# Performance work log

Hardware: AMD Instinct MI355X
Metric: run time of the kernel (lower is better)

Reference implementation:

```python
import jax, jax.numpy as jnp
import numpy as np

VOCAB = 100000
DIM = 128
B = 16384
C_MAX = 10
K_NEG = 5


def setup_inputs() -> dict:
    key = jax.random.key(0)
    k1, k2, k3, k4, k5, k6 = jax.random.split(key, 6)
    bound = 0.5 / DIM
    return {
        "target_words": jax.random.randint(k1, (B,), 0, VOCAB),
        "context_words": jax.random.randint(k2, (B, C_MAX), 0, VOCAB),
        "context_lens": jax.random.randint(k3, (B,), 0, C_MAX + 1),
        "negative_words": jax.random.randint(k4, (B, K_NEG), 0, VOCAB),
        # input embeddings init: uniform(-0.5/dim, 0.5/dim); output init zeros in the
        # original, but we use small random values so gradients/scores are non-trivial.
        "in_emb": jax.random.uniform(k5, (VOCAB, DIM), jnp.float32, -bound, bound),
        "out_emb": jax.random.normal(k6, (VOCAB, DIM), jnp.float32) * 0.01,
    }


def reference(target_words, context_words, context_lens, negative_words, in_emb, out_emb):
    t = in_emb[target_words]                      # (B, D)
    c = out_emb[context_words]                    # (B, C, D)
    n = out_emb[negative_words]                   # (B, K, D)

    pos_scores = jnp.einsum("bd,bcd->bc", t, c)   # (B, C)
    neg_scores = jnp.einsum("bd,bkd->bk", t, n)   # (B, K)

    mask = (jnp.arange(C_MAX)[None, :] < context_lens[:, None]).astype(t.dtype)
    lens = context_lens.astype(t.dtype)
    has_ctx = lens > 0

    # per-sample mean of -logsigmoid over valid contexts; skip samples with 0 contexts
    pos_per = -jnp.sum(jax.nn.log_sigmoid(pos_scores) * mask, axis=1)
    pos_per = jnp.where(has_ctx, pos_per / jnp.maximum(lens, 1.0), 0.0)

    neg_per = -jnp.mean(jax.nn.log_sigmoid(-neg_scores), axis=1)
    neg_per = jnp.where(has_ctx, neg_per, 0.0)    # original `continue` skips negatives too

    positive_loss = jnp.sum(pos_per) / B
    negative_loss = jnp.sum(neg_per) / B
    return positive_loss, negative_loss
```

## Files before the change

### kernel.cpp

```cpp
#include <hip/hip_runtime.h>
#include <math.h>
#include <stdint.h>

#define VOCAB 100000
#define DIM   128
#define BATCH 16384
#define CMAX  10
#define KNEG  5

typedef float f32x4 __attribute__((ext_vector_type(4)));

__device__ __forceinline__ float log_sigmoid(float x) {
    return fminf(x, 0.0f) - log1pf(expf(-fabsf(x)));
}

#define DPP_ADD_STEP(v, ctrl)                                                  \
    v += __int_as_float(__builtin_amdgcn_update_dpp(                           \
        0, __float_as_int(v), (ctrl), 0xF, 0xF, false))

__device__ __forceinline__ float dpp_reduce32_to_lane31(float v) {
    DPP_ADD_STEP(v, 0x111);
    DPP_ADD_STEP(v, 0x112);
    DPP_ADD_STEP(v, 0x114);
    DPP_ADD_STEP(v, 0x118);
    DPP_ADD_STEP(v, 0x142);
    return v;
}

__global__ __launch_bounds__(256) void score_loss_kernel(
    const int*   __restrict__ tgt,
    const int*   __restrict__ ctx,
    const int*   __restrict__ lens,
    const int*   __restrict__ neg,
    const float* __restrict__ in_emb,
    const float* __restrict__ out_emb,
    float2*      __restrict__ per_sample,
    float*       __restrict__ out)
{
    const int tid  = threadIdx.x;
    const int lane = tid & 63;
    const int sub  = lane & 31;
    const int half = lane >> 5;
    const int b    = (blockIdx.x * 256 + tid) >> 6;

    if (blockIdx.x == 0 && tid < 2) out[tid] = 0.0f;

    const int len    = lens[b];
    const int t_word = tgt[b];
    int words[8];
#pragma unroll
    for (int jj = 0; jj < 8; ++jj) {
        const int j = half * 8 + jj;
        if (j < CMAX)             words[jj] = ctx[b * CMAX + j];
        else if (j < CMAX + KNEG) words[jj] = neg[b * KNEG + (j - CMAX)];
        else                      words[jj] = 0;
    }

    asm volatile("s_waitcnt vmcnt(0)" ::: "memory");

    const uint32_t sub16 = (uint32_t)sub * 16u;
    f32x4 tv;
    {
        uint32_t off = (uint32_t)t_word * (DIM * 4u) + sub16;
        asm volatile("global_load_dwordx4 %0, %1, %2"
                     : "=v"(tv) : "v"(off), "s"(in_emb));
    }
    f32x4 rv[8];
#pragma unroll
    for (int jj = 0; jj < 8; ++jj) {
        uint32_t off = (uint32_t)words[jj] * (DIM * 4u) + sub16;
        asm volatile("global_load_dwordx4 %0, %1, %2"
                     : "=v"(rv[jj]) : "v"(off), "s"(out_emb));
    }

    float p[8];
#pragma unroll
    for (int jj = 0; jj < 8; ++jj) {
        asm volatile("s_waitcnt vmcnt(%[cnt])"
                     : "+v"(rv[jj]), "+v"(tv)
                     : [cnt] "i"(7 - jj)
                     : "memory");
        float d = tv.x * rv[jj].x + tv.y * rv[jj].y +
                  tv.z * rv[jj].z + tv.w * rv[jj].w;
        p[jj] = dpp_reduce32_to_lane31(d);
    }

    float bc[8];
#pragma unroll
    for (int jj = 0; jj < 8; ++jj) bc[jj] = __shfl(p[jj], 31, 32);

    const int sel = sub & 7;
    float a0 = (sel & 1) ? bc[1] : bc[0];
    float a1 = (sel & 1) ? bc[3] : bc[2];
    float a2 = (sel & 1) ? bc[5] : bc[4];
    float a3 = (sel & 1) ? bc[7] : bc[6];
    float b0 = (sel & 2) ? a1 : a0;
    float b1 = (sel & 2) ? a3 : a2;
    float s  = (sel & 4) ? b1 : b0;

    const int  j        = half * 8 + sel;
    const bool neg_slot = (j >= CMAX) && (j < CMAX + KNEG);
    const bool active   = (sub < 8);

    float v    = log_sigmoid(neg_slot ? -s : s);
    float posc = (active && j < len)    ? v : 0.0f;
    float negc = (active && neg_slot)   ? v : 0.0f;

    posc += __shfl_xor(posc, 1, 64);
    posc += __shfl_xor(posc, 2, 64);
    posc += __shfl_xor(posc, 4, 64);
    posc += __shfl_xor(posc, 32, 64);
    negc += __shfl_xor(negc, 1, 64);
    negc += __shfl_xor(negc, 2, 64);
    negc += __shfl_xor(negc, 4, 64);
    negc += __shfl_xor(negc, 32, 64);

    if (lane == 0) {
        float2 r;
        if (len > 0) {
            r.x = -posc / (float)len;
            r.y = -negc * (1.0f / KNEG);
        } else {
            r.x = 0.0f;
            r.y = 0.0f;
        }
        per_sample[b] = r;
    }
}

__global__ __launch_bounds__(256) void reduce_kernel(
    const float2* __restrict__ per_sample,
    float*        __restrict__ out)
{
    const int tid = threadIdx.x;
    const int b   = blockIdx.x * 256 + tid;

    const float2 pr = per_sample[b];
    float pos = pr.x;
    float neg = pr.y;

#pragma unroll
    for (int m = 32; m >= 1; m >>= 1) {
        pos += __shfl_xor(pos, m, 64);
        neg += __shfl_xor(neg, m, 64);
    }
    __shared__ float s_pos[4];
    __shared__ float s_neg[4];
    const int wave = tid >> 6;
    if ((tid & 63) == 0) { s_pos[wave] = pos; s_neg[wave] = neg; }
    __syncthreads();
    if (tid == 0) {
        float ps = s_pos[0] + s_pos[1] + s_pos[2] + s_pos[3];
        float ns = s_neg[0] + s_neg[1] + s_neg[2] + s_neg[3];
        atomicAdd(&out[0], ps * (1.0f / BATCH));
        atomicAdd(&out[1], ns * (1.0f / BATCH));
    }
}

extern "C" void kernel_launch(void* const* d_in, const int* in_sizes, int n_in,
                              void* d_out, int out_size, void* d_ws, size_t ws_size,
                              hipStream_t stream) {
    const int*   tgt     = (const int*)  d_in[0];
    const int*   ctx     = (const int*)  d_in[1];
    const int*   lens    = (const int*)  d_in[2];
    const int*   neg     = (const int*)  d_in[3];
    const float* in_emb  = (const float*)d_in[4];
    const float* out_emb = (const float*)d_in[5];
    float* out          = (float*)d_out;
    float2* per_sample  = (float2*)d_ws;

    score_loss_kernel<<<BATCH / 4, 256, 0, stream>>>(
        tgt, ctx, lens, neg, in_emb, out_emb, per_sample, out);

    reduce_kernel<<<BATCH / 256, 256, 0, stream>>>(per_sample, out);
}
```

Measured before the change: 132.0 us.

## Gather only valid context rows and use full-wave dwordx2 row loads

Each wave now loads only the len valid context rows plus the negatives. Samples with zero contexts skip all loads, since the reference zeroes their loss anyway. Previously the wave always fetched all ten context rows and the five negatives. Each embedding row is now read by the whole 64-lane wave with dwordx2 loads, and the dot product is reduced with a 64-lane DPP chain instead of two half-waves using dwordx4. The aim is to cut gather traffic on masked rows, in exchange for a single full wait on all loads instead of the staggered per-row waits and a longer reduction per row.

```diff
diff --git a/kernel.cpp b/kernel.cpp
--- a/kernel.cpp
+++ b/kernel.cpp
@@ -7,8 +7,9 @@
 #define BATCH 16384
 #define CMAX  10
 #define KNEG  5
+#define RMAX  (CMAX + KNEG)
 
-typedef float f32x4 __attribute__((ext_vector_type(4)));
+typedef float f32x2 __attribute__((ext_vector_type(2)));
 
 __device__ __forceinline__ float log_sigmoid(float x) {
     return fminf(x, 0.0f) - log1pf(expf(-fabsf(x)));
@@ -18,12 +19,13 @@
     v += __int_as_float(__builtin_amdgcn_update_dpp(                           \
         0, __float_as_int(v), (ctrl), 0xF, 0xF, false))
 
-__device__ __forceinline__ float dpp_reduce32_to_lane31(float v) {
+__device__ __forceinline__ float dpp_reduce64_to_lane63(float v) {
     DPP_ADD_STEP(v, 0x111);
     DPP_ADD_STEP(v, 0x112);
     DPP_ADD_STEP(v, 0x114);
     DPP_ADD_STEP(v, 0x118);
     DPP_ADD_STEP(v, 0x142);
+    DPP_ADD_STEP(v, 0x143);
     return v;
 }
 
@@ -39,93 +41,97 @@
 {
     const int tid  = threadIdx.x;
     const int lane = tid & 63;
-    const int sub  = lane & 31;
-    const int half = lane >> 5;
     const int b    = (blockIdx.x * 256 + tid) >> 6;
 
     if (blockIdx.x == 0 && tid < 2) out[tid] = 0.0f;
 
-    const int len    = lens[b];
-    const int t_word = tgt[b];
-    int words[8];
+    const int len = lens[b];
+    float2 res; res.x = 0.0f; res.y = 0.0f;
+
+    if (len > 0) {
+        const int R      = len + KNEG;
+        const int t_word = tgt[b];
+
+        int words[RMAX];
 #pragma unroll
-    for (int jj = 0; jj < 8; ++jj) {
-        const int j = half * 8 + jj;
-        if (j < CMAX)             words[jj] = ctx[b * CMAX + j];
-        else if (j < CMAX + KNEG) words[jj] = neg[b * KNEG + (j - CMAX)];
-        else                      words[jj] = 0;
+        for (int j = 0; j < RMAX; ++j) {
+            if (j < R) {
+                const int cj = (j < CMAX) ? j : (CMAX - 1);
+                int nj = j - len;
+                nj = (nj < 0) ? 0 : ((nj > KNEG - 1) ? (KNEG - 1) : nj);
+                words[j] = (j < len) ? ctx[b * CMAX + cj]
+                                     : neg[b * KNEG + nj];
+            }
+        }
+
+        const uint32_t lane8 = (uint32_t)lane * 8u;
+        f32x2 tv;
+        asm volatile("global_load_dwordx2 %0, %1, %2"
+                     : "=v"(tv)
+                     : "v"((uint32_t)t_word * (DIM * 4u) + lane8),
+                       "s"(in_emb));
+        f32x2 rv[RMAX];
+#pragma unroll
+        for (int j = 0; j < RMAX; ++j) {
+            if (j < R) {
+                asm volatile("global_load_dwordx2 %0, %1, %2"
+                             : "=v"(rv[j])
+                             : "v"((uint32_t)words[j] * (DIM * 4u) + lane8),
+                               "s"(out_emb));
+            }
+        }
+        asm volatile("s_waitcnt vmcnt(0)" ::: "memory");
+        __builtin_amdgcn_sched_barrier(0);
+
+        float bc[RMAX];
+#pragma unroll
+        for (int j = 0; j < RMAX; ++j) bc[j] = 0.0f;
+#pragma unroll
+        for (int j = 0; j < RMAX; ++j) {
+            if (j < R) {
+                float d = tv.x * rv[j].x + tv.y * rv[j].y;
+                float s = dpp_reduce64_to_lane63(d);
+                bc[j] = __shfl(s, 63, 64);
+            }
+        }
+
+        const int sel = lane & 15;
+        float m0 = (sel & 1) ? bc[1]  : bc[0];
+        float m1 = (sel & 1) ? bc[3]  : bc[2];
+        float m2 = (sel & 1) ? bc[5]  : bc[4];
+        float m3 = (sel & 1) ? bc[7]  : bc[6];
+        float m4 = (sel & 1) ? bc[9]  : bc[8];
+        float m5 = (sel & 1) ? bc[11] : bc[10];
+        float m6 = (sel & 1) ? bc[13] : bc[12];
+        float m7 = (sel & 1) ? 0.0f   : bc[14];
+        float n0 = (sel & 2) ? m1 : m0;
+        float n1 = (sel & 2) ? m3 : m2;
+        float n2 = (sel & 2) ? m5 : m4;
+        float n3 = (sel & 2) ? m7 : m6;
+        float q0 = (sel & 4) ? n1 : n0;
+        float q1 = (sel & 4) ? n3 : n2;
+        float sv = (sel & 8) ? q1 : q0;
+
+        const bool active = (lane < 16) && (sel < R);
+        const bool is_neg = (sel >= len);
+        float v = log_sigmoid(is_neg ? -sv : sv);
+        float posc = (active && !is_neg) ? v : 0.0f;
+        float negc = (active &&  is_neg) ? v : 0.0f;
+
+        posc += __shfl_xor(posc, 1, 64);
+        posc += __shfl_xor(posc, 2, 64);
+        posc += __shfl_xor(posc, 4, 64);
+        posc += __shfl_xor(posc, 8, 64);
+        negc += __shfl_xor(negc, 1, 64);
+        negc += __shfl_xor(negc, 2, 64);
+        negc += __shfl_xor(negc, 4, 64);
+        negc += __shfl_xor(negc, 8, 64);
+
+        res.x = -posc / (float)len;
+        res.y = -negc * (1.0f / KNEG);
     }
 
-    asm volatile("s_waitcnt vmcnt(0)" ::: "memory");
-
-    const uint32_t sub16 = (uint32_t)sub * 16u;
-    f32x4 tv;
-    {
-        uint32_t off = (uint32_t)t_word * (DIM * 4u) + sub16;
-        asm volatile("global_load_dwordx4 %0, %1, %2"
-                     : "=v"(tv) : "v"(off), "s"(in_emb));
-    }
-    f32x4 rv[8];
-#pragma unroll
-    for (int jj = 0; jj < 8; ++jj) {
-        uint32_t off = (uint32_t)words[jj] * (DIM * 4u) + sub16;
-        asm volatile("global_load_dwordx4 %0, %1, %2"
-                     : "=v"(rv[jj]) : "v"(off), "s"(out_emb));
-    }
-
-    float p[8];
-#pragma unroll
-    for (int jj = 0; jj < 8; ++jj) {
-        asm volatile("s_waitcnt vmcnt(%[cnt])"
-                     : "+v"(rv[jj]), "+v"(tv)
-                     : [cnt] "i"(7 - jj)
-                     : "memory");
-        float d = tv.x * rv[jj].x + tv.y * rv[jj].y +
-                  tv.z * rv[jj].z + tv.w * rv[jj].w;
-        p[jj] = dpp_reduce32_to_lane31(d);
-    }
-
-    float bc[8];
-#pragma unroll
-    for (int jj = 0; jj < 8; ++jj) bc[jj] = __shfl(p[jj], 31, 32);
-
-    const int sel = sub & 7;
-    float a0 = (sel & 1) ? bc[1] : bc[0];
-    float a1 = (sel & 1) ? bc[3] : bc[2];
-    float a2 = (sel & 1) ? bc[5] : bc[4];
-    float a3 = (sel & 1) ? bc[7] : bc[6];
-    float b0 = (sel & 2) ? a1 : a0;
-    float b1 = (sel & 2) ? a3 : a2;
-    float s  = (sel & 4) ? b1 : b0;
-
-    const int  j        = half * 8 + sel;
-    const bool neg_slot = (j >= CMAX) && (j < CMAX + KNEG);
-    const bool active   = (sub < 8);
-
-    float v    = log_sigmoid(neg_slot ? -s : s);
-    float posc = (active && j < len)    ? v : 0.0f;
-    float negc = (active && neg_slot)   ? v : 0.0f;
-
-    posc += __shfl_xor(posc, 1, 64);
-    posc += __shfl_xor(posc, 2, 64);
-    posc += __shfl_xor(posc, 4, 64);
-    posc += __shfl_xor(posc, 32, 64);
-    negc += __shfl_xor(negc, 1, 64);
-    negc += __shfl_xor(negc, 2, 64);
-    negc += __shfl_xor(negc, 4, 64);
-    negc += __shfl_xor(negc, 32, 64);
-
-    if (lane == 0) {
-        float2 r;
-        if (len > 0) {
-            r.x = -posc / (float)len;
-            r.y = -negc * (1.0f / KNEG);
-        } else {
-            r.x = 0.0f;
-            r.y = 0.0f;
-        }
-        per_sample[b] = r;
-    }
+    if (lane == 0) per_sample[b] = res;
 }
 
 __global__ __launch_bounds__(256) void reduce_kernel(
```

After: 253.4 us. 92.0% more time.

## Process four samples per wave with double-buffered gather loads

Applied to the files above, without the earlier changes.

Each wave now handles four samples instead of one and keeps two sets of embedding-row loads in flight, consuming one set while the next is issued. Index loads become wave-uniform, so they can go through the scalar path. Unused context slots are redirected to a negative-word row that is already being fetched, so those loads should hit cache. The grid shrinks by a factor of four, which trades occupancy-based latency hiding for explicit in-wave pipelining and raises register pressure.

```diff
diff --git a/kernel.cpp b/kernel.cpp
--- a/kernel.cpp
+++ b/kernel.cpp
@@ -26,6 +26,103 @@
     DPP_ADD_STEP(v, 0x142);
     return v;
 }
+
+
+#define ISSUE(twv, w, tv, rv)                                                  \
+    {                                                                          \
+        asm volatile("global_load_dwordx4 %0, %1, %2"                          \
+                     : "=v"(tv)                                                \
+                     : "v"((uint32_t)(twv) * 512u + sub16), "s"(in_emb));      \
+        asm volatile("global_load_dwordx4 %0, %1, %2"                          \
+                     : "=v"(rv[0])                                             \
+                     : "v"((uint32_t)(w)[0] * 512u + sub16), "s"(out_emb));    \
+        asm volatile("global_load_dwordx4 %0, %1, %2"                          \
+                     : "=v"(rv[1])                                             \
+                     : "v"((uint32_t)(w)[1] * 512u + sub16), "s"(out_emb));    \
+        asm volatile("global_load_dwordx4 %0, %1, %2"                          \
+                     : "=v"(rv[2])                                             \
+                     : "v"((uint32_t)(w)[2] * 512u + sub16), "s"(out_emb));    \
+        asm volatile("global_load_dwordx4 %0, %1, %2"                          \
+                     : "=v"(rv[3])                                             \
+                     : "v"((uint32_t)(w)[3] * 512u + sub16), "s"(out_emb));    \
+        asm volatile("global_load_dwordx4 %0, %1, %2"                          \
+                     : "=v"(rv[4])                                             \
+                     : "v"((uint32_t)(w)[4] * 512u + sub16), "s"(out_emb));    \
+        asm volatile("global_load_dwordx4 %0, %1, %2"                          \
+                     : "=v"(rv[5])                                             \
+                     : "v"((uint32_t)(w)[5] * 512u + sub16), "s"(out_emb));    \
+        asm volatile("global_load_dwordx4 %0, %1, %2"                          \
+                     : "=v"(rv[6])                                             \
+                     : "v"((uint32_t)(w)[6] * 512u + sub16), "s"(out_emb));    \
+        asm volatile("global_load_dwordx4 %0, %1, %2"                          \
+                     : "=v"(rv[7])                                             \
+                     : "v"((uint32_t)(w)[7] * 512u + sub16), "s"(out_emb));    \
+    }
+
+#define WAITN(n, tv, rv)                                                       \
+    asm volatile("s_waitcnt vmcnt(" #n ")"                                     \
+                 : "+v"(tv), "+v"(rv[0]), "+v"(rv[1]), "+v"(rv[2]),            \
+                   "+v"(rv[3]), "+v"(rv[4]), "+v"(rv[5]), "+v"(rv[6]),         \
+                   "+v"(rv[7])                                                 \
+                 :                                                             \
+                 : "memory")
+
+#define BUILD_WORDS(i, w)                                                      \
+    {                                                                          \
+        _Pragma("unroll")                                                      \
+        for (int jj = 0; jj < 8; ++jj) {                                       \
+            const int w0 = (jj < len_[i]) ? cw_[i][jj] : nw_[i][0];            \
+            int w1;                                                            \
+            if (jj < 2)      w1 = ((8 + jj) < len_[i]) ? cw_[i][8 + jj]        \
+                                                       : nw_[i][0];            \
+            else if (jj < 7) w1 = nw_[i][jj - 2];                              \
+            else             w1 = nw_[i][0];                                   \
+            (w)[jj] = half ? w1 : w0;                                          \
+        }                                                                      \
+    }
+
+#define CONSUME(tv, rv, len, res)                                              \
+    {                                                                          \
+        float p[8];                                                            \
+        _Pragma("unroll")                                                      \
+        for (int jj = 0; jj < 8; ++jj) {                                       \
+            float d = tv.x * rv[jj].x + tv.y * rv[jj].y +                      \
+                      tv.z * rv[jj].z + tv.w * rv[jj].w;                       \
+            p[jj] = dpp_reduce32_to_lane31(d);                                 \
+        }                                                                      \
+        float bc[8];                                                           \
+        _Pragma("unroll")                                                      \
+        for (int jj = 0; jj < 8; ++jj) bc[jj] = __shfl(p[jj], 31, 32);         \
+        const int sel = sub & 7;                                               \
+        float a0 = (sel & 1) ? bc[1] : bc[0];                                  \
+        float a1 = (sel & 1) ? bc[3] : bc[2];                                  \
+        float a2 = (sel & 1) ? bc[5] : bc[4];                                  \
+        float a3 = (sel & 1) ? bc[7] : bc[6];                                  \
+        float b0_ = (sel & 2) ? a1 : a0;                                       \
+        float b1_ = (sel & 2) ? a3 : a2;                                       \
+        float sv = (sel & 4) ? b1_ : b0_;                                      \
+        const int  j        = half * 8 + sel;                                  \
+        const bool neg_slot = (j >= CMAX) && (j < CMAX + KNEG);                \
+        const bool active   = (sub < 8);                                       \
+        float v    = log_sigmoid(neg_slot ? -sv : sv);                         \
+        float posc = (active && j < (len)) ? v : 0.0f;                         \
+        float negc = (active && neg_slot)  ? v : 0.0f;                         \
+        posc += __shfl_xor(posc, 1, 64);                                       \
+        posc += __shfl_xor(posc, 2, 64);                                       \
+        posc += __shfl_xor(posc, 4, 64);                                       \
+        posc += __shfl_xor(posc, 32, 64);                                      \
+        negc += __shfl_xor(negc, 1, 64);                                       \
+        negc += __shfl_xor(negc, 2, 64);                                       \
+        negc += __shfl_xor(negc, 4, 64);                                       \
+        negc += __shfl_xor(negc, 32, 64);                                      \
+        if ((len) > 0) {                                                       \
+            res.x = -posc / (float)(len);                                      \
+            res.y = -negc * (1.0f / KNEG);                                     \
+        } else {                                                               \
+            res.x = 0.0f;                                                      \
+            res.y = 0.0f;                                                      \
+        }                                                                      \
+    }
 
 __global__ __launch_bounds__(256) void score_loss_kernel(
     const int*   __restrict__ tgt,
@@ -41,90 +138,53 @@
     const int lane = tid & 63;
     const int sub  = lane & 31;
     const int half = lane >> 5;
-    const int b    = (blockIdx.x * 256 + tid) >> 6;
+    const int wid  = __builtin_amdgcn_readfirstlane((blockIdx.x * 256 + tid) >> 6);
+    const int b0   = wid * 4;
 
     if (blockIdx.x == 0 && tid < 2) out[tid] = 0.0f;
 
-    const int len    = lens[b];
-    const int t_word = tgt[b];
-    int words[8];
-#pragma unroll
-    for (int jj = 0; jj < 8; ++jj) {
-        const int j = half * 8 + jj;
-        if (j < CMAX)             words[jj] = ctx[b * CMAX + j];
-        else if (j < CMAX + KNEG) words[jj] = neg[b * KNEG + (j - CMAX)];
-        else                      words[jj] = 0;
-    }
+    int len_[4], tw_[4];
+    int cw_[4][CMAX], nw_[4][KNEG];
+#pragma unroll
+    for (int i = 0; i < 4; ++i) {
+        len_[i] = lens[b0 + i];
+        tw_[i]  = tgt[b0 + i];
+#pragma unroll
+        for (int c = 0; c < CMAX; ++c) cw_[i][c] = ctx[(b0 + i) * CMAX + c];
+#pragma unroll
+        for (int k = 0; k < KNEG; ++k) nw_[i][k] = neg[(b0 + i) * KNEG + k];
+    }
+
+    const uint32_t sub16 = (uint32_t)sub * 16u;
 
     asm volatile("s_waitcnt vmcnt(0)" ::: "memory");
 
-    const uint32_t sub16 = (uint32_t)sub * 16u;
-    f32x4 tv;
-    {
-        uint32_t off = (uint32_t)t_word * (DIM * 4u) + sub16;
-        asm volatile("global_load_dwordx4 %0, %1, %2"
-                     : "=v"(tv) : "v"(off), "s"(in_emb));
-    }
-    f32x4 rv[8];
-#pragma unroll
-    for (int jj = 0; jj < 8; ++jj) {
-        uint32_t off = (uint32_t)words[jj] * (DIM * 4u) + sub16;
-        asm volatile("global_load_dwordx4 %0, %1, %2"
-                     : "=v"(rv[jj]) : "v"(off), "s"(out_emb));
-    }
-
-    float p[8];
-#pragma unroll
-    for (int jj = 0; jj < 8; ++jj) {
-        asm volatile("s_waitcnt vmcnt(%[cnt])"
-                     : "+v"(rv[jj]), "+v"(tv)
-                     : [cnt] "i"(7 - jj)
-                     : "memory");
-        float d = tv.x * rv[jj].x + tv.y * rv[jj].y +
-                  tv.z * rv[jj].z + tv.w * rv[jj].w;
-        p[jj] = dpp_reduce32_to_lane31(d);
-    }
-
-    float bc[8];
-#pragma unroll
-    for (int jj = 0; jj < 8; ++jj) bc[jj] = __shfl(p[jj], 31, 32);
-
-    const int sel = sub & 7;
-    float a0 = (sel & 1) ? bc[1] : bc[0];
-    float a1 = (sel & 1) ? bc[3] : bc[2];
-    float a2 = (sel & 1) ? bc[5] : bc[4];
-    float a3 = (sel & 1) ? bc[7] : bc[6];
-    float b0 = (sel & 2) ? a1 : a0;
-    float b1 = (sel & 2) ? a3 : a2;
-    float s  = (sel & 4) ? b1 : b0;
-
-    const int  j        = half * 8 + sel;
-    const bool neg_slot = (j >= CMAX) && (j < CMAX + KNEG);
-    const bool active   = (sub < 8);
-
-    float v    = log_sigmoid(neg_slot ? -s : s);
-    float posc = (active && j < len)    ? v : 0.0f;
-    float negc = (active && neg_slot)   ? v : 0.0f;
-
-    posc += __shfl_xor(posc, 1, 64);
-    posc += __shfl_xor(posc, 2, 64);
-    posc += __shfl_xor(posc, 4, 64);
-    posc += __shfl_xor(posc, 32, 64);
-    negc += __shfl_xor(negc, 1, 64);
-    negc += __shfl_xor(negc, 2, 64);
-    negc += __shfl_xor(negc, 4, 64);
-    negc += __shfl_xor(negc, 32, 64);
+    f32x4 tvA, rvA[8], tvB, rvB[8];
+    int   wA[8], wB[8];
+    float2 res0, res1, res2, res3;
+
+    BUILD_WORDS(0, wA); ISSUE(tw_[0], wA, tvA, rvA);
+    BUILD_WORDS(1, wB); ISSUE(tw_[1], wB, tvB, rvB);
+
+    WAITN(9, tvA, rvA);
+    CONSUME(tvA, rvA, len_[0], res0);
+    BUILD_WORDS(2, wA); ISSUE(tw_[2], wA, tvA, rvA);
+
+    WAITN(9, tvB, rvB);
+    CONSUME(tvB, rvB, len_[1], res1);
+    BUILD_WORDS(3, wB); ISSUE(tw_[3], wB, tvB, rvB);
+
+    WAITN(9, tvA, rvA);
+    CONSUME(tvA, rvA, len_[2], res2);
+
+    WAITN(0, tvB, rvB);
+    CONSUME(tvB, rvB, len_[3], res3);
 
     if (lane == 0) {
-        float2 r;
-        if (len > 0) {
-            r.x = -posc / (float)len;
-            r.y = -negc * (1.0f / KNEG);
-        } else {
-            r.x = 0.0f;
-            r.y = 0.0f;
-        }
-        per_sample[b] = r;
+        per_sample[b0 + 0] = res0;
+        per_sample[b0 + 1] = res1;
+        per_sample[b0 + 2] = res2;
+        per_sample[b0 + 3] = res3;
     }
 }
 
@@ -169,7 +229,7 @@
     float* out          = (float*)d_out;
     float2* per_sample  = (float2*)d_ws;
 
-    score_loss_kernel<<<BATCH / 4, 256, 0, stream>>>(
+    score_loss_kernel<<<BATCH / 16, 256, 0, stream>>>(
         tgt, ctx, lens, neg, in_emb, out_emb, per_sample, out);
 
     reduce_kernel<<<BATCH / 256, 256, 0, stream>>>(per_sample, out);
```

Result: faster. 127.4 us (-3.5%).
